# Kernel tuning notes

Hardware: AMD Instinct MI355X
Metric: run time of the kernel (lower is better)

## Reference

```python
import jax, jax.numpy as jnp
import numpy as np

B, C, H, W, NH = 4, 96, 256, 256, 4


def setup_inputs() -> dict:
    key = jax.random.key(0)
    ks = jax.random.split(key, 8)
    s = 0.05  # keep pre-activations well-scaled
    return {
        "x": jax.random.normal(ks[0], (B, C, H, W), jnp.float32),
        "ff": jax.random.normal(ks[1], (B, C, H, W), jnp.float32),
        "w_q": jax.random.normal(ks[2], (C, C, 1, 1), jnp.float32) * s,
        "w_kv": jax.random.normal(ks[3], (2 * C, C, 1, 1), jnp.float32) * s,
        "w_q_dw": jax.random.normal(ks[4], (C, 1, 3, 3), jnp.float32) * s,
        "w_kv_dw": jax.random.normal(ks[5], (2 * C, 1, 3, 3), jnp.float32) * s,
        "w_out": jax.random.normal(ks[6], (C, C, 1, 1), jnp.float32) * s,
        "temperature": jnp.ones((NH, 1, 1), jnp.float32),
    }


def _conv1x1(x, w):
    # pointwise conv == channel GEMM; w: [O, I, 1, 1]
    return jnp.einsum('bchw,oc->bohw', x, w[:, :, 0, 0])


def _dwconv3(x, w):
    # depthwise 3x3, padding=1; w: [C, 1, 3, 3]
    return jax.lax.conv_general_dilated(
        x, w, window_strides=(1, 1), padding='SAME',
        feature_group_count=x.shape[1],
        dimension_numbers=('NCHW', 'OIHW', 'NCHW'))


def _l2norm(t, eps=1e-12):
    # L2-normalize along last (HW) axis, torch F.normalize semantics
    n = jnp.sqrt(jnp.sum(t * t, axis=-1, keepdims=True))
    return t / jnp.maximum(n, eps)


def reference(x, ff, w_q, w_kv, w_q_dw, w_kv_dw, w_out, temperature):
    b, c, h, w = x.shape
    q = _dwconv3(_conv1x1(ff, w_q), w_q_dw)          # [B,C,H,W]
    kv = _dwconv3(_conv1x1(x, w_kv), w_kv_dw)        # [B,2C,H,W]
    k, v = jnp.split(kv, 2, axis=1)

    def heads(t):
        return t.reshape(b, NH, c // NH, h * w)       # [B,nh,c,HW]

    q = _l2norm(heads(q))
    k = _l2norm(heads(k))
    v = heads(v)
    # channel-wise (transposed) attention: [B,nh,c,c]
    attn = jax.nn.softmax(jnp.einsum('bhcn,bhdn->bhcd', q, k) * temperature, axis=-1)
    o = jnp.einsum('bhcd,bhdn->bhcn', attn, v).reshape(b, c, h, w)
    return _conv1x1(o, w_out)
```

## Files before the change

kernel.cpp:

```cpp
#include <hip/hip_runtime.h>
#include <hip/hip_bf16.h>
#include <hip/hip_fp16.h>

typedef unsigned int u32;
typedef unsigned short u16;
typedef _Float16 f16;

static constexpr int HWn = 65536;

typedef __attribute__((ext_vector_type(8))) f16 f16x8;
typedef __attribute__((ext_vector_type(2))) f16 f16x2;
typedef __attribute__((ext_vector_type(4))) float f32x4;

__device__ __forceinline__ float h2f(u16 u) {
    union { u16 s; f16 h; } z; z.s = u; return (float)z.h;
}
__device__ __forceinline__ u16 f2h(float f) {
    union { u16 s; f16 h; } z; z.h = (f16)f; return z.s;
}
__device__ __forceinline__ u32 pack2h(float a, float b) {
    union { u32 i; f16 h[2]; } z; z.h[0] = (f16)a; z.h[1] = (f16)b; return z.i;
}
__device__ __forceinline__ float hlo(u32 u) {
    union { u32 i; f16 h[2]; } z; z.i = u; return (float)z.h[0];
}
__device__ __forceinline__ float hhi(u32 u) {
    union { u32 i; f16 h[2]; } z; z.i = u; return (float)z.h[1];
}
__device__ __forceinline__ float sq2h(u32 a) {
    const float l = hlo(a), h = hhi(a);
    return fmaf(l, l, h * h);
}

#if defined(__has_builtin)
#if __has_builtin(__builtin_amdgcn_fdot2)
#define HAS_FDOT2 1
#endif
#endif
__device__ __forceinline__ float fdot2a(u32 a, u32 b, float c) {
#ifdef HAS_FDOT2
    union { u32 i; f16x2 h; } A, B; A.i = a; B.i = b;
    return __builtin_amdgcn_fdot2(A.h, B.h, c, false);
#else
    return fmaf(hlo(a), hlo(b), fmaf(hhi(a), hhi(b), c));
#endif
}

__device__ __forceinline__ int xoff(int px, int icb) {
    return px * 128 + (((icb ^ (px & 7) ^ ((px >> 3) & 7))) << 3);
}

__global__ __launch_bounds__(256) void k_prep_w(
    const float* __restrict__ wq, const float* __restrict__ wkv,
    u16* __restrict__ wf)
{
    const int i = blockIdx.x * 256 + threadIdx.x;
    if (i >= 288 * 96) return;
    const int row = i / 96, ic = i % 96;
    const float w = (row < 96) ? wq[row * 96 + ic] : wkv[(row - 96) * 96 + ic];
    wf[i] = f2h(w);
}

__global__ __launch_bounds__(256, 3) void k_conv_mfma(
    const float* __restrict__ ff, const float* __restrict__ x,
    const u16* __restrict__ wf,
    u16* __restrict__ qpre, u16* __restrict__ kvpre)
{
    const int b = blockIdx.z, sec = blockIdx.y;
    const int pxb = blockIdx.x * 256;
    const int tid = threadIdx.x;

    __shared__ __align__(16) u16 xs[16384];

    const float* src = (sec == 0 ? ff : x) + (size_t)b * 96 * HWn;
    const int icq = (tid >> 4) * 2;
    const int pxs = (tid & 15) * 8;
    const int lane = tid & 63;
    const int wv = tid >> 6;
    const int oc0 = (wv >> 1) * 48;
    const int pxw = (wv & 1) * 64;
    const int lr = lane & 15, lg = lane >> 4;

    float4 L[12];

    auto issue = [&](int px0) {
        #pragma unroll
        for (int p = 0; p < 3; ++p) {
            const float* rp0 = src + (size_t)(p * 32 + icq) * HWn + px0 + pxs;
            const float* rp1 = rp0 + HWn;
            L[p * 4 + 0] = *reinterpret_cast<const float4*>(rp0);
            L[p * 4 + 1] = *reinterpret_cast<const float4*>(rp0 + 4);
            L[p * 4 + 2] = *reinterpret_cast<const float4*>(rp1);
            L[p * 4 + 3] = *reinterpret_cast<const float4*>(rp1 + 4);
        }
    };
    auto stage = [&]() {
        #pragma unroll
        for (int p = 0; p < 3; ++p) {
            const int ic = p * 32 + icq;
            const int icb = ic >> 3, icl = ic & 7;
            const float e0[8] = {L[p*4+0].x, L[p*4+0].y, L[p*4+0].z, L[p*4+0].w,
                                 L[p*4+1].x, L[p*4+1].y, L[p*4+1].z, L[p*4+1].w};
            const float e1[8] = {L[p*4+2].x, L[p*4+2].y, L[p*4+2].z, L[p*4+2].w,
                                 L[p*4+3].x, L[p*4+3].y, L[p*4+3].z, L[p*4+3].w};
            #pragma unroll
            for (int j = 0; j < 8; ++j) {
                const int o = xoff(pxs + j, icb) + icl;
                *reinterpret_cast<u32*>(&xs[o]) = pack2h(e0[j], e1[j]);
            }
        }
    };
    auto compute = [&](int px0) {
        const int npass = (sec == 0) ? 1 : 2;
        #pragma unroll 1
        for (int kvs = 0; kvs < npass; ++kvs) {
            const u16* wh = wf + ((sec == 0) ? 0 : (96 + kvs * 96)) * 96;
            u16* dst = (sec == 0) ? (qpre + (size_t)b * 96 * HWn)
                                  : (kvpre + (size_t)b * 192 * HWn + (size_t)kvs * 96 * HWn);
            f32x4 acc[3][4];
            #pragma unroll
            for (int m = 0; m < 3; ++m)
                #pragma unroll
                for (int n = 0; n < 4; ++n)
                    acc[m][n] = (f32x4){0.f, 0.f, 0.f, 0.f};

            #pragma unroll 1
            for (int kt = 0; kt < 3; ++kt) {
                const int kb = kt * 32;
                f16x8 B[4];
                #pragma unroll
                for (int n = 0; n < 4; ++n)
                    B[n] = *(const f16x8*)(xs + xoff(pxw + n * 16 + lr, (kb >> 3) + lg));
                f16x8 A[3];
                #pragma unroll
                for (int m = 0; m < 3; ++m)
                    A[m] = *(const f16x8*)(wh + (oc0 + m * 16 + lr) * 96 + kb + lg * 8);
                #pragma unroll
                for (int m = 0; m < 3; ++m)
                    #pragma unroll
                    for (int n = 0; n < 4; ++n)
                        acc[m][n] = __builtin_amdgcn_mfma_f32_16x16x32_f16(A[m], B[n], acc[m][n], 0, 0, 0);
            }

            #pragma unroll
            for (int m = 0; m < 3; ++m) {
                #pragma unroll
                for (int i = 0; i < 4; ++i) {
                    const int oc = oc0 + m * 16 + lg * 4 + i;
                    u16* drow = dst + (size_t)oc * HWn + px0;
                    #pragma unroll
                    for (int n = 0; n < 4; ++n)
                        drow[pxw + n * 16 + lr] = f2h(acc[m][n][i]);
                }
            }
        }
    };

    issue(pxb);
    stage();
    __syncthreads();
    issue(pxb + 128);
    compute(pxb);
    __syncthreads();
    stage();
    __syncthreads();
    compute(pxb + 128);
}

__device__ __forceinline__ void row3tap(
    const uint4 m, u32 lv, u32 rv, u32 w01, u32 w2z, float* a)
{
    const u32 P0 = m.x, P1 = m.y, P2 = m.z, P3 = m.w;
    const u32 s0 = (lv >> 16) | (P0 << 16);
    const u32 s1 = (P0 >> 16) | (P1 << 16);
    const u32 s2 = (P1 >> 16) | (P2 << 16);
    const u32 s3 = (P2 >> 16) | (P3 << 16);
    const u32 s4 = (P3 >> 16) | (rv << 16);
    a[0] = fdot2a(w2z, s1, fdot2a(w01, s0, a[0]));
    a[1] = fdot2a(w2z, P1, fdot2a(w01, P0, a[1]));
    a[2] = fdot2a(w2z, s2, fdot2a(w01, s1, a[2]));
    a[3] = fdot2a(w2z, P2, fdot2a(w01, P1, a[3]));
    a[4] = fdot2a(w2z, s3, fdot2a(w01, s2, a[4]));
    a[5] = fdot2a(w2z, P3, fdot2a(w01, P2, a[5]));
    a[6] = fdot2a(w2z, s4, fdot2a(w01, s3, a[6]));
    a[7] = fdot2a(w2z, rv, fdot2a(w01, P3, a[7]));
}

__global__ __launch_bounds__(512) void k_dw_qk(
    const u16* __restrict__ qpre, const u16* __restrict__ kvpre,
    const float* __restrict__ wqdw, const float* __restrict__ wkvdw,
    float* __restrict__ ssq, float* __restrict__ Sg)
{
    const int bid = blockIdx.x;
    const int wg = (bid & 7) * 256 + (bid >> 3);
    const int b = wg >> 9;
    const int rem = wg & 511;
    const int y = rem >> 1;
    const int tx = (rem & 1) * 128;
    const int tid = threadIdx.x;
    const int lane = tid & 63;
    const int pq = tid >> 4;
    const int chunk = tid & 15;
    const int x0l = chunk * 8;
    const int xg = tx + x0l;

    const bool vr0 = (y > 0), vr2 = (y < 255);
    const bool le = (chunk == 0) && (xg > 0);
    const bool re = (chunk == 15) && (xg + 8 < 256);

    __shared__ __align__(16) u16 qs[96][136];
    __shared__ __align__(16) u16 ks[96][136];

    auto addr = [&](int it, const u16*& src, const float*& wp, int& c, int& seg) {
        const int p = it * 32 + pq;
        if (p < 96) { c = p;      src = qpre  + ((size_t)(b * 96 + c)) * HWn;  wp = wqdw  + c * 9; seg = 0; }
        else        { c = p - 96; src = kvpre + ((size_t)(b * 192 + c)) * HWn; wp = wkvdw + c * 9; seg = 1; }
    };
    auto issue = [&](const u16* src, uint4* m, u32* el, u32* er) {
        const uint4 z = make_uint4(0u, 0u, 0u, 0u);
        const u16* r0 = src + (y - 1) * 256 + xg;
        const u16* r1 = r0 + 256;
        const u16* r2 = r1 + 256;
        m[0] = vr0 ? *reinterpret_cast<const uint4*>(r0) : z;
        m[1] = *reinterpret_cast<const uint4*>(r1);
        m[2] = vr2 ? *reinterpret_cast<const uint4*>(r2) : z;
        el[0] = (le && vr0) ? ((u32)r0[-1] << 16) : 0u;  er[0] = (re && vr0) ? (u32)r0[8] : 0u;
        el[1] = le ? ((u32)r1[-1] << 16) : 0u;           er[1] = re ? (u32)r1[8] : 0u;
        el[2] = (le && vr2) ? ((u32)r2[-1] << 16) : 0u;  er[2] = (re && vr2) ? (u32)r2[8] : 0u;
    };

    const u16* srcC; const float* wpC; int cC, segC;
    addr(0, srcC, wpC, cC, segC);
    uint4 mcur[3]; u32 elc[3], erc[3];
    issue(srcC, mcur, elc, erc);

    #pragma unroll 1
    for (int it = 0; it < 6; ++it) {
        const u16* srcN; const float* wpN; int cN, segN;
        uint4 mnx[3]; u32 eln[3], ern[3];
        if (it < 5) {
            addr(it + 1, srcN, wpN, cN, segN);
            issue(srcN, mnx, eln, ern);
        }

        float a[8] = {0.f, 0.f, 0.f, 0.f, 0.f, 0.f, 0.f, 0.f};
        #pragma unroll
        for (int r = 0; r < 3; ++r) {
            const u32 w01 = pack2h(wpC[r * 3 + 0], wpC[r * 3 + 1]);
            const u32 w2z = pack2h(wpC[r * 3 + 2], 0.f);
            const u32 lvn = __shfl((int)mcur[r].w, (lane - 1) & 63);
            const u32 rvn = __shfl((int)mcur[r].x, (lane + 1) & 63);
            const u32 lv = (chunk == 0)  ? elc[r] : lvn;
            const u32 rv = (chunk == 15) ? erc[r] : rvn;
            row3tap(mcur[r], lv, rv, w01, w2z, a);
        }

        const uint4 o = make_uint4(pack2h(a[0], a[1]), pack2h(a[2], a[3]),
                                   pack2h(a[4], a[5]), pack2h(a[6], a[7]));
        if (segC == 0) *reinterpret_cast<uint4*>(&qs[cC][x0l]) = o;
        else           *reinterpret_cast<uint4*>(&ks[cC][x0l]) = o;

        if (it < 5) {
            #pragma unroll
            for (int r = 0; r < 3; ++r) { mcur[r] = mnx[r]; elc[r] = eln[r]; erc[r] = ern[r]; }
            wpC = wpN; cC = cN; segC = segN;
        }
    }
    __syncthreads();

    if (tid < 384) {
        const int half = tid >= 192;
        const int r = tid - half * 192;
        const uint4* rr = reinterpret_cast<const uint4*>(
            (r < 96 ? &qs[r][0] : &ks[r - 96][0]) + half * 64);
        float s = 0.f;
        #pragma unroll
        for (int pch = 0; pch < 8; ++pch) {
            const uint4 a = rr[pch];
            s += sq2h(a.x) + sq2h(a.y) + sq2h(a.z) + sq2h(a.w);
        }
        atomicAdd(ssq + b * 192 + r, s);
    }

    {
        const int w = tid >> 6;
        const int h = w & 3, mt = w >> 2;
        const int lr2 = lane & 15, lg2 = lane >> 4;
        const int ar = h * 24 + min(mt * 16 + lr2, 23);
        f32x4 acc2[2];
        acc2[0] = (f32x4){0.f, 0.f, 0.f, 0.f};
        acc2[1] = (f32x4){0.f, 0.f, 0.f, 0.f};
        #pragma unroll
        for (int ks4 = 0; ks4 < 4; ++ks4) {
            const f16x8 A = *(const f16x8*)(&qs[ar][ks4 * 32 + lg2 * 8]);
            #pragma unroll
            for (int nt = 0; nt < 2; ++nt) {
                const int bc = h * 24 + min(nt * 16 + lr2, 23);
                const f16x8 B = *(const f16x8*)(&ks[bc][ks4 * 32 + lg2 * 8]);
                acc2[nt] = __builtin_amdgcn_mfma_f32_16x16x32_f16(A, B, acc2[nt], 0, 0, 0);
            }
        }
        #pragma unroll
        for (int nt = 0; nt < 2; ++nt) {
            const int col = nt * 16 + lr2;
            #pragma unroll
            for (int reg = 0; reg < 4; ++reg) {
                const int row24 = mt * 16 + lg2 * 4 + reg;
                if (row24 < 24 && col < 24)
                    atomicAdd(Sg + b * 2304 + h * 576 + row24 * 24 + col, acc2[nt][reg]);
            }
        }
    }
}

__global__ __launch_bounds__(256) void k_attn_fold(
    const float* __restrict__ ssq, const float* __restrict__ S,
    const float* __restrict__ temp, const float* __restrict__ w_out,
    u16* __restrict__ mf)
{
    const int b = blockIdx.x;
    const int tid = threadIdx.x;
    __shared__ float rq[96], rk[96], att[2304];

    if (tid < 96) {
        rq[tid] = 1.f / fmaxf(sqrtf(ssq[b * 192 + tid]), 1e-12f);
    } else if (tid < 192) {
        const int c = tid - 96;
        rk[c] = 1.f / fmaxf(sqrtf(ssq[b * 192 + 96 + c]), 1e-12f);
    }
    __syncthreads();

    if (tid < 96) {
        const int h = tid / 24, i = tid % 24;
        const float tmp = temp[h];
        const float rqi = rq[h * 24 + i];
        float l[24];
        float m = -1e30f;
        #pragma unroll
        for (int j = 0; j < 24; ++j) {
            l[j] = S[b * 2304 + (h * 24 + i) * 24 + j] * rqi * rk[h * 24 + j] * tmp;
            m = fmaxf(m, l[j]);
        }
        float ssum = 0.f;
        #pragma unroll
        for (int j = 0; j < 24; ++j) { l[j] = expf(l[j] - m); ssum += l[j]; }
        const float inv = 1.f / ssum;
        #pragma unroll
        for (int j = 0; j < 24; ++j) att[(h * 24 + i) * 24 + j] = l[j] * inv;
    }
    __syncthreads();

    for (int k = 0; k < 36; ++k) {
        const int id = k * 256 + tid;
        const int dg = id / 96, oc = id % 96;
        const int h = dg / 24, d24 = dg % 24;
        float s = 0.f;
        #pragma unroll
        for (int i = 0; i < 24; ++i) {
            s += w_out[oc * 96 + h * 24 + i] * att[(h * 24 + i) * 24 + d24];
        }
        mf[b * 9216 + oc * 96 + dg] = f2h(s);
    }
}

__global__ __launch_bounds__(256, 4) void k_v_out(
    const u16* __restrict__ kvpre, const float* __restrict__ wkvdw,
    const u16* __restrict__ mf, float* __restrict__ out)
{
    const int bid = blockIdx.x;
    const int wg = (bid & 7) * 256 + (bid >> 3);
    const int b = wg >> 9;
    const int rem = wg & 511;
    const int y = rem >> 1;
    const int tx = (rem & 1) * 128;
    const int tid = threadIdx.x;
    const int lane = tid & 63;
    const int slot = tid >> 4;
    const int chunk = tid & 15;
    const int x0l = chunk * 8;
    const int xg = tx + x0l;

    const bool vr0 = (y > 0), vr2 = (y < 255);
    const bool le = (chunk == 0) && (xg > 0);
    const bool re = (chunk == 15) && (xg + 8 < 256);

    __shared__ __align__(16) u16 xt[16384];

    auto issue = [&](int it, uint4* m0, uint4* m1, u32* e0l, u32* e0r, u32* e1l, u32* e1r) {
        const int dg = (it * 16 + slot) * 2;
        const u16* s0 = kvpre + ((size_t)(b * 192 + 96 + dg)) * HWn + (y - 1) * 256 + xg;
        const u16* s1 = s0 + HWn;
        const uint4 z = make_uint4(0u, 0u, 0u, 0u);
        m0[0] = vr0 ? *reinterpret_cast<const uint4*>(s0)       : z;
        m0[1] =       *reinterpret_cast<const uint4*>(s0 + 256);
        m0[2] = vr2 ? *reinterpret_cast<const uint4*>(s0 + 512) : z;
        m1[0] = vr0 ? *reinterpret_cast<const uint4*>(s1)       : z;
        m1[1] =       *reinterpret_cast<const uint4*>(s1 + 256);
        m1[2] = vr2 ? *reinterpret_cast<const uint4*>(s1 + 512) : z;
        e0l[0] = (le && vr0) ? ((u32)s0[-1] << 16) : 0u;   e0r[0] = (re && vr0) ? (u32)s0[8] : 0u;
        e0l[1] = le ? ((u32)s0[255] << 16) : 0u;           e0r[1] = re ? (u32)s0[264] : 0u;
        e0l[2] = (le && vr2) ? ((u32)s0[511] << 16) : 0u;  e0r[2] = (re && vr2) ? (u32)s0[520] : 0u;
        e1l[0] = (le && vr0) ? ((u32)s1[-1] << 16) : 0u;   e1r[0] = (re && vr0) ? (u32)s1[8] : 0u;
        e1l[1] = le ? ((u32)s1[255] << 16) : 0u;           e1r[1] = re ? (u32)s1[264] : 0u;
        e1l[2] = (le && vr2) ? ((u32)s1[511] << 16) : 0u;  e1r[2] = (re && vr2) ? (u32)s1[520] : 0u;
    };

    uint4 m0c[3], m1c[3]; u32 e0lc[3], e0rc[3], e1lc[3], e1rc[3];
    issue(0, m0c, m1c, e0lc, e0rc, e1lc, e1rc);

    #pragma unroll 1
    for (int it = 0; it < 3; ++it) {
        uint4 m0n[3], m1n[3]; u32 e0ln[3], e0rn[3], e1ln[3], e1rn[3];
        if (it < 2) issue(it + 1, m0n, m1n, e0ln, e0rn, e1ln, e1rn);

        const int dg = (it * 16 + slot) * 2;
        const float* wp0 = wkvdw + (96 + dg) * 9;
        const float* wp1 = wp0 + 9;

        float a0[8] = {0.f, 0.f, 0.f, 0.f, 0.f, 0.f, 0.f, 0.f};
        float a1[8] = {0.f, 0.f, 0.f, 0.f, 0.f, 0.f, 0.f, 0.f};
        #pragma unroll
        for (int r = 0; r < 3; ++r) {
            {
                const u32 w01 = pack2h(wp0[r * 3 + 0], wp0[r * 3 + 1]);
                const u32 w2z = pack2h(wp0[r * 3 + 2], 0.f);
                const u32 lvn = __shfl((int)m0c[r].w, (lane - 1) & 63);
                const u32 rvn = __shfl((int)m0c[r].x, (lane + 1) & 63);
                const u32 lv = (chunk == 0)  ? e0lc[r] : lvn;
                const u32 rv = (chunk == 15) ? e0rc[r] : rvn;
                row3tap(m0c[r], lv, rv, w01, w2z, a0);
            }
            {
                const u32 w01 = pack2h(wp1[r * 3 + 0], wp1[r * 3 + 1]);
                const u32 w2z = pack2h(wp1[r * 3 + 2], 0.f);
                const u32 lvn = __shfl((int)m1c[r].w, (lane - 1) & 63);
                const u32 rvn = __shfl((int)m1c[r].x, (lane + 1) & 63);
                const u32 lv = (chunk == 0)  ? e1lc[r] : lvn;
                const u32 rv = (chunk == 15) ? e1rc[r] : rvn;
                row3tap(m1c[r], lv, rv, w01, w2z, a1);
            }
        }

        const int icb = dg >> 3, icl = dg & 7;
        #pragma unroll
        for (int j = 0; j < 8; ++j) {
            *reinterpret_cast<u32*>(&xt[xoff(x0l + j, icb) + icl]) = pack2h(a0[j], a1[j]);
        }

        if (it < 2) {
            #pragma unroll
            for (int r = 0; r < 3; ++r) {
                m0c[r] = m0n[r]; m1c[r] = m1n[r];
                e0lc[r] = e0ln[r]; e0rc[r] = e0rn[r];
                e1lc[r] = e1ln[r]; e1rc[r] = e1rn[r];
            }
        }
    }
    __syncthreads();

    const u16* mh = mf + b * 9216;
    const int wv = tid >> 6;
    const int oc0 = (wv >> 1) * 48;
    const int pxw = (wv & 1) * 64;
    const int lr = lane & 15, lg = lane >> 4;

    f32x4 acc[3][4];
    #pragma unroll
    for (int m = 0; m < 3; ++m)
        #pragma unroll
        for (int n = 0; n < 4; ++n)
            acc[m][n] = (f32x4){0.f, 0.f, 0.f, 0.f};

    #pragma unroll 1
    for (int kt = 0; kt < 3; ++kt) {
        const int kb = kt * 32;
        f16x8 B[4];
        #pragma unroll
        for (int n = 0; n < 4; ++n)
            B[n] = *(const f16x8*)(xt + xoff(pxw + n * 16 + lr, (kb >> 3) + lg));
        f16x8 A[3];
        #pragma unroll
        for (int m = 0; m < 3; ++m)
            A[m] = *(const f16x8*)(mh + (oc0 + m * 16 + lr) * 96 + kb + lg * 8);
        #pragma unroll
        for (int m = 0; m < 3; ++m)
            #pragma unroll
            for (int n = 0; n < 4; ++n)
                acc[m][n] = __builtin_amdgcn_mfma_f32_16x16x32_f16(A[m], B[n], acc[m][n], 0, 0, 0);
    }

    #pragma unroll
    for (int m = 0; m < 3; ++m) {
        #pragma unroll
        for (int i = 0; i < 4; ++i) {
            const int oc = oc0 + m * 16 + lg * 4 + i;
            float* drow = out + ((size_t)(b * 96 + oc)) * HWn + y * 256 + tx;
            #pragma unroll
            for (int n = 0; n < 4; ++n)
                drow[pxw + n * 16 + lr] = acc[m][n][i];
        }
    }
}

extern "C" void kernel_launch(void* const* d_in, const int* in_sizes, int n_in,
                              void* d_out, int out_size, void* d_ws, size_t ws_size,
                              hipStream_t stream) {
    (void)in_sizes; (void)n_in; (void)out_size; (void)ws_size;
    const float* x      = (const float*)d_in[0];
    const float* ff     = (const float*)d_in[1];
    const float* w_q    = (const float*)d_in[2];
    const float* w_kv   = (const float*)d_in[3];
    const float* w_q_dw = (const float*)d_in[4];
    const float* w_kv_dw= (const float*)d_in[5];
    const float* w_out  = (const float*)d_in[6];
    const float* temp   = (const float*)d_in[7];
    float* out = (float*)d_out;

    char* ws = (char*)d_ws;
    u16* qpre   = (u16*)(ws);
    u16* kvpre  = (u16*)(ws + 50331648);
    float* ssq  = (float*)(ws + 150994944);
    float* S    = (float*)(ws + 150998016);
    u16* wf     = (u16*)(ws + 151034880);
    u16* mf     = (u16*)(ws + 151090176);

    hipMemsetAsync(ws + 150994944, 0, 3072 + 36864, stream);

    k_prep_w<<<108, 256, 0, stream>>>(w_q, w_kv, wf);
    k_conv_mfma<<<dim3(256, 2, 4), 256, 0, stream>>>(ff, x, wf, qpre, kvpre);
    k_dw_qk<<<dim3(2048), 512, 0, stream>>>(qpre, kvpre, w_q_dw, w_kv_dw, ssq, S);
    k_attn_fold<<<4, 256, 0, stream>>>(ssq, S, temp, w_out, mf);
    k_v_out<<<dim3(2048), 256, 0, stream>>>(kvpre, w_kv_dw, mf, out);
}
```

Before: 257.0 us.

## Shrink conv and depthwise tiles, drop software prefetch, raise occupancy

The pointwise-conv kernel now processes 64 pixels per block instead of two 128-pixel halves with register prefetch. It stages fp32 inputs into half the shared memory and launches four times as many blocks with a higher occupancy hint. The depthwise/QK kernel now handles a 64-wide tile with 64 channels per iteration instead of 128-wide with 32. It drops the next-iteration prefetch and doubles the grid. The intent is to hide latency with more resident waves rather than explicit pipelining, at the cost of more blocks, more atomics on ssq/S and more halo reloads.

```diff
diff --git a/kernel.cpp b/kernel.cpp
--- a/kernel.cpp
+++ b/kernel.cpp
@@ -61,110 +61,85 @@
     wf[i] = f2h(w);
 }
 
-__global__ __launch_bounds__(256, 3) void k_conv_mfma(
+__global__ __launch_bounds__(256, 6) void k_conv_mfma(
     const float* __restrict__ ff, const float* __restrict__ x,
     const u16* __restrict__ wf,
     u16* __restrict__ qpre, u16* __restrict__ kvpre)
 {
     const int b = blockIdx.z, sec = blockIdx.y;
-    const int pxb = blockIdx.x * 256;
+    const int px0 = blockIdx.x * 64;
     const int tid = threadIdx.x;
 
-    __shared__ __align__(16) u16 xs[16384];
+    __shared__ __align__(16) u16 xs[8192];
 
     const float* src = (sec == 0 ? ff : x) + (size_t)b * 96 * HWn;
-    const int icq = (tid >> 4) * 2;
-    const int pxs = (tid & 15) * 8;
+
+    const int ics = tid >> 3;
+    const int pxs = (tid & 7) * 8;
+    #pragma unroll
+    for (int p = 0; p < 3; ++p) {
+        const int ic = p * 32 + ics;
+        const float* rp = src + (size_t)ic * HWn + px0 + pxs;
+        const float4 a0 = *reinterpret_cast<const float4*>(rp);
+        const float4 a1 = *reinterpret_cast<const float4*>(rp + 4);
+        const int icb = ic >> 3, icl = ic & 7;
+        const float e[8] = {a0.x, a0.y, a0.z, a0.w, a1.x, a1.y, a1.z, a1.w};
+        #pragma unroll
+        for (int j = 0; j < 8; ++j)
+            xs[xoff(pxs + j, icb) + icl] = f2h(e[j]);
+    }
+    __syncthreads();
+
     const int lane = tid & 63;
     const int wv = tid >> 6;
     const int oc0 = (wv >> 1) * 48;
-    const int pxw = (wv & 1) * 64;
+    const int pxw = (wv & 1) * 32;
     const int lr = lane & 15, lg = lane >> 4;
 
-    float4 L[12];
-
-    auto issue = [&](int px0) {
-        #pragma unroll
-        for (int p = 0; p < 3; ++p) {
-            const float* rp0 = src + (size_t)(p * 32 + icq) * HWn + px0 + pxs;
-            const float* rp1 = rp0 + HWn;
-            L[p * 4 + 0] = *reinterpret_cast<const float4*>(rp0);
-            L[p * 4 + 1] = *reinterpret_cast<const float4*>(rp0 + 4);
-            L[p * 4 + 2] = *reinterpret_cast<const float4*>(rp1);
-            L[p * 4 + 3] = *reinterpret_cast<const float4*>(rp1 + 4);
-        }
-    };
-    auto stage = [&]() {
-        #pragma unroll
-        for (int p = 0; p < 3; ++p) {
-            const int ic = p * 32 + icq;
-            const int icb = ic >> 3, icl = ic & 7;
-            const float e0[8] = {L[p*4+0].x, L[p*4+0].y, L[p*4+0].z, L[p*4+0].w,
-                                 L[p*4+1].x, L[p*4+1].y, L[p*4+1].z, L[p*4+1].w};
-            const float e1[8] = {L[p*4+2].x, L[p*4+2].y, L[p*4+2].z, L[p*4+2].w,
-                                 L[p*4+3].x, L[p*4+3].y, L[p*4+3].z, L[p*4+3].w};
-            #pragma unroll
-            for (int j = 0; j < 8; ++j) {
-                const int o = xoff(pxs + j, icb) + icl;
-                *reinterpret_cast<u32*>(&xs[o]) = pack2h(e0[j], e1[j]);
-            }
-        }
-    };
-    auto compute = [&](int px0) {
-        const int npass = (sec == 0) ? 1 : 2;
+    const int npass = (sec == 0) ? 1 : 2;
+    #pragma unroll 1
+    for (int kvs = 0; kvs < npass; ++kvs) {
+        const u16* wh = wf + ((sec == 0) ? 0 : (96 + kvs * 96)) * 96;
+        u16* dst = (sec == 0) ? (qpre + (size_t)b * 96 * HWn)
+                              : (kvpre + (size_t)b * 192 * HWn + (size_t)kvs * 96 * HWn);
+
+        f32x4 acc[3][2];
+        #pragma unroll
+        for (int m = 0; m < 3; ++m)
+            #pragma unroll
+            for (int n = 0; n < 2; ++n)
+                acc[m][n] = (f32x4){0.f, 0.f, 0.f, 0.f};
+
         #pragma unroll 1
-        for (int kvs = 0; kvs < npass; ++kvs) {
-            const u16* wh = wf + ((sec == 0) ? 0 : (96 + kvs * 96)) * 96;
-            u16* dst = (sec == 0) ? (qpre + (size_t)b * 96 * HWn)
-                                  : (kvpre + (size_t)b * 192 * HWn + (size_t)kvs * 96 * HWn);
-            f32x4 acc[3][4];
+        for (int kt = 0; kt < 3; ++kt) {
+            const int kb = kt * 32;
+            f16x8 B[2];
+            #pragma unroll
+            for (int n = 0; n < 2; ++n)
+                B[n] = *(const f16x8*)(xs + xoff(pxw + n * 16 + lr, (kb >> 3) + lg));
+            f16x8 A[3];
+            #pragma unroll
+            for (int m = 0; m < 3; ++m)
+                A[m] = *(const f16x8*)(wh + (oc0 + m * 16 + lr) * 96 + kb + lg * 8);
             #pragma unroll
             for (int m = 0; m < 3; ++m)
                 #pragma unroll
-                for (int n = 0; n < 4; ++n)
-                    acc[m][n] = (f32x4){0.f, 0.f, 0.f, 0.f};
-
-            #pragma unroll 1
-            for (int kt = 0; kt < 3; ++kt) {
-                const int kb = kt * 32;
-                f16x8 B[4];
+                for (int n = 0; n < 2; ++n)
+                    acc[m][n] = __builtin_amdgcn_mfma_f32_16x16x32_f16(A[m], B[n], acc[m][n], 0, 0, 0);
+        }
+
+        #pragma unroll
+        for (int m = 0; m < 3; ++m) {
+            #pragma unroll
+            for (int i = 0; i < 4; ++i) {
+                const int oc = oc0 + m * 16 + lg * 4 + i;
+                u16* drow = dst + (size_t)oc * HWn + px0;
                 #pragma unroll
-                for (int n = 0; n < 4; ++n)
-                    B[n] = *(const f16x8*)(xs + xoff(pxw + n * 16 + lr, (kb >> 3) + lg));
-                f16x8 A[3];
-                #pragma unroll
-                for (int m = 0; m < 3; ++m)
-                    A[m] = *(const f16x8*)(wh + (oc0 + m * 16 + lr) * 96 + kb + lg * 8);
-                #pragma unroll
-                for (int m = 0; m < 3; ++m)
-                    #pragma unroll
-                    for (int n = 0; n < 4; ++n)
-                        acc[m][n] = __builtin_amdgcn_mfma_f32_16x16x32_f16(A[m], B[n], acc[m][n], 0, 0, 0);
-            }
-
-            #pragma unroll
-            for (int m = 0; m < 3; ++m) {
-                #pragma unroll
-                for (int i = 0; i < 4; ++i) {
-                    const int oc = oc0 + m * 16 + lg * 4 + i;
-                    u16* drow = dst + (size_t)oc * HWn + px0;
-                    #pragma unroll
-                    for (int n = 0; n < 4; ++n)
-                        drow[pxw + n * 16 + lr] = f2h(acc[m][n][i]);
-                }
-            }
-        }
-    };
-
-    issue(pxb);
-    stage();
-    __syncthreads();
-    issue(pxb + 128);
-    compute(pxb);
-    __syncthreads();
-    stage();
-    __syncthreads();
-    compute(pxb + 128);
+                for (int n = 0; n < 2; ++n)
+                    drow[pxw + n * 16 + lr] = f2h(acc[m][n][i]);
+            }
+        }
+    }
 }
 
 __device__ __forceinline__ void row3tap(
@@ -186,100 +161,80 @@
     a[7] = fdot2a(w2z, rv, fdot2a(w01, P3, a[7]));
 }
 
-__global__ __launch_bounds__(512) void k_dw_qk(
+__global__ __launch_bounds__(512, 8) void k_dw_qk(
     const u16* __restrict__ qpre, const u16* __restrict__ kvpre,
     const float* __restrict__ wqdw, const float* __restrict__ wkvdw,
     float* __restrict__ ssq, float* __restrict__ Sg)
 {
     const int bid = blockIdx.x;
-    const int wg = (bid & 7) * 256 + (bid >> 3);
-    const int b = wg >> 9;
-    const int rem = wg & 511;
-    const int y = rem >> 1;
-    const int tx = (rem & 1) * 128;
+    const int wg = (bid & 7) * 512 + (bid >> 3);
+    const int b = wg >> 10;
+    const int rem = wg & 1023;
+    const int y = rem >> 2;
+    const int tx = (rem & 3) * 64;
     const int tid = threadIdx.x;
     const int lane = tid & 63;
-    const int pq = tid >> 4;
-    const int chunk = tid & 15;
+    const int pq = tid >> 3;
+    const int chunk = tid & 7;
     const int x0l = chunk * 8;
     const int xg = tx + x0l;
 
     const bool vr0 = (y > 0), vr2 = (y < 255);
     const bool le = (chunk == 0) && (xg > 0);
-    const bool re = (chunk == 15) && (xg + 8 < 256);
-
-    __shared__ __align__(16) u16 qs[96][136];
-    __shared__ __align__(16) u16 ks[96][136];
-
-    auto addr = [&](int it, const u16*& src, const float*& wp, int& c, int& seg) {
-        const int p = it * 32 + pq;
+    const bool re = (chunk == 7) && (xg + 8 < 256);
+
+    __shared__ __align__(16) u16 qs[96][72];
+    __shared__ __align__(16) u16 ks[96][72];
+
+    #pragma unroll 1
+    for (int it = 0; it < 3; ++it) {
+        const int p = it * 64 + pq;
+        const u16* src; const float* wp; int c, seg;
         if (p < 96) { c = p;      src = qpre  + ((size_t)(b * 96 + c)) * HWn;  wp = wqdw  + c * 9; seg = 0; }
         else        { c = p - 96; src = kvpre + ((size_t)(b * 192 + c)) * HWn; wp = wkvdw + c * 9; seg = 1; }
-    };
-    auto issue = [&](const u16* src, uint4* m, u32* el, u32* er) {
-        const uint4 z = make_uint4(0u, 0u, 0u, 0u);
+
         const u16* r0 = src + (y - 1) * 256 + xg;
         const u16* r1 = r0 + 256;
         const u16* r2 = r1 + 256;
+        const uint4 z = make_uint4(0u, 0u, 0u, 0u);
+        uint4 m[3];
         m[0] = vr0 ? *reinterpret_cast<const uint4*>(r0) : z;
         m[1] = *reinterpret_cast<const uint4*>(r1);
         m[2] = vr2 ? *reinterpret_cast<const uint4*>(r2) : z;
+        u32 el[3], er[3];
         el[0] = (le && vr0) ? ((u32)r0[-1] << 16) : 0u;  er[0] = (re && vr0) ? (u32)r0[8] : 0u;
         el[1] = le ? ((u32)r1[-1] << 16) : 0u;           er[1] = re ? (u32)r1[8] : 0u;
         el[2] = (le && vr2) ? ((u32)r2[-1] << 16) : 0u;  er[2] = (re && vr2) ? (u32)r2[8] : 0u;
-    };
-
-    const u16* srcC; const float* wpC; int cC, segC;
-    addr(0, srcC, wpC, cC, segC);
-    uint4 mcur[3]; u32 elc[3], erc[3];
-    issue(srcC, mcur, elc, erc);
-
-    #pragma unroll 1
-    for (int it = 0; it < 6; ++it) {
-        const u16* srcN; const float* wpN; int cN, segN;
-        uint4 mnx[3]; u32 eln[3], ern[3];
-        if (it < 5) {
-            addr(it + 1, srcN, wpN, cN, segN);
-            issue(srcN, mnx, eln, ern);
-        }
 
         float a[8] = {0.f, 0.f, 0.f, 0.f, 0.f, 0.f, 0.f, 0.f};
         #pragma unroll
         for (int r = 0; r < 3; ++r) {
-            const u32 w01 = pack2h(wpC[r * 3 + 0], wpC[r * 3 + 1]);
-            const u32 w2z = pack2h(wpC[r * 3 + 2], 0.f);
-            const u32 lvn = __shfl((int)mcur[r].w, (lane - 1) & 63);
-            const u32 rvn = __shfl((int)mcur[r].x, (lane + 1) & 63);
-            const u32 lv = (chunk == 0)  ? elc[r] : lvn;
-            const u32 rv = (chunk == 15) ? erc[r] : rvn;
-            row3tap(mcur[r], lv, rv, w01, w2z, a);
+            const u32 w01 = pack2h(wp[r * 3 + 0], wp[r * 3 + 1]);
+            const u32 w2z = pack2h(wp[r * 3 + 2], 0.f);
+            const u32 lvn = __shfl((int)m[r].w, (lane - 1) & 63);
+            const u32 rvn = __shfl((int)m[r].x, (lane + 1) & 63);
+            const u32 lv = (chunk == 0) ? el[r] : lvn;
+            const u32 rv = (chunk == 7) ? er[r] : rvn;
+            row3tap(m[r], lv, rv, w01, w2z, a);
         }
 
         const uint4 o = make_uint4(pack2h(a[0], a[1]), pack2h(a[2], a[3]),
                                    pack2h(a[4], a[5]), pack2h(a[6], a[7]));
-        if (segC == 0) *reinterpret_cast<uint4*>(&qs[cC][x0l]) = o;
-        else           *reinterpret_cast<uint4*>(&ks[cC][x0l]) = o;
-
-        if (it < 5) {
-            #pragma unroll
-            for (int r = 0; r < 3; ++r) { mcur[r] = mnx[r]; elc[r] = eln[r]; erc[r] = ern[r]; }
-            wpC = wpN; cC = cN; segC = segN;
-        }
+        if (seg == 0) *reinterpret_cast<uint4*>(&qs[c][x0l]) = o;
+        else          *reinterpret_cast<uint4*>(&ks[c][x0l]) = o;
     }
     __syncthreads();
 
-    if (tid < 384) {
-        const int half = tid >= 192;
-        const int r = tid - half * 192;
+    if (tid < 192) {
         const uint4* rr = reinterpret_cast<const uint4*>(
-            (r < 96 ? &qs[r][0] : &ks[r - 96][0]) + half * 64);
+            tid < 96 ? &qs[tid][0] : &ks[tid - 96][0]);
         float s = 0.f;
         #pragma unroll
         for (int pch = 0; pch < 8; ++pch) {
             const uint4 a = rr[pch];
             s += sq2h(a.x) + sq2h(a.y) + sq2h(a.z) + sq2h(a.w);
         }
-        atomicAdd(ssq + b * 192 + r, s);
+        atomicAdd(ssq + b * 192 + tid, s);
     }
 
     {
@@ -291,7 +246,7 @@
         acc2[0] = (f32x4){0.f, 0.f, 0.f, 0.f};
         acc2[1] = (f32x4){0.f, 0.f, 0.f, 0.f};
         #pragma unroll
-        for (int ks4 = 0; ks4 < 4; ++ks4) {
+        for (int ks4 = 0; ks4 < 2; ++ks4) {
             const f16x8 A = *(const f16x8*)(&qs[ar][ks4 * 32 + lg2 * 8]);
             #pragma unroll
             for (int nt = 0; nt < 2; ++nt) {
@@ -527,8 +482,8 @@
     hipMemsetAsync(ws + 150994944, 0, 3072 + 36864, stream);
 
     k_prep_w<<<108, 256, 0, stream>>>(w_q, w_kv, wf);
-    k_conv_mfma<<<dim3(256, 2, 4), 256, 0, stream>>>(ff, x, wf, qpre, kvpre);
-    k_dw_qk<<<dim3(2048), 512, 0, stream>>>(qpre, kvpre, w_q_dw, w_kv_dw, ssq, S);
+    k_conv_mfma<<<dim3(1024, 2, 4), 256, 0, stream>>>(ff, x, wf, qpre, kvpre);
+    k_dw_qk<<<dim3(4096), 512, 0, stream>>>(qpre, kvpre, w_q_dw, w_kv_dw, ssq, S);
     k_attn_fold<<<4, 256, 0, stream>>>(ssq, S, temp, w_out, mf);
     k_v_out<<<dim3(2048), 256, 0, stream>>>(kvpre, w_kv_dw, mf, out);
 }
```

Measured after the change: 301.6 us. 1.17x slower.

## Process batches sequentially and fuse attention fold into the output kernel

Applied to the files above, without the earlier changes.

The host now loops over the batch, launching conv, depthwise/QK and V-output kernels once per batch. The q/kv intermediate buffers shrink to one batch's worth so they can stay resident in cache between stages. The separate softmax/fold kernel is removed: every k_v_out block recomputes the softmax and the w_out·attn matrix into shared memory. The trade-off is redundant per-block fold work, more and smaller launches, and extra LDS use, with a lower occupancy hint in launch bounds.

```diff
diff --git a/kernel.cpp b/kernel.cpp
--- a/kernel.cpp
+++ b/kernel.cpp
@@ -62,17 +62,17 @@
 }
 
 __global__ __launch_bounds__(256, 3) void k_conv_mfma(
-    const float* __restrict__ ff, const float* __restrict__ x,
+    const float* __restrict__ ffb, const float* __restrict__ xb,
     const u16* __restrict__ wf,
     u16* __restrict__ qpre, u16* __restrict__ kvpre)
 {
-    const int b = blockIdx.z, sec = blockIdx.y;
+    const int sec = blockIdx.y;
     const int pxb = blockIdx.x * 256;
     const int tid = threadIdx.x;
 
     __shared__ __align__(16) u16 xs[16384];
 
-    const float* src = (sec == 0 ? ff : x) + (size_t)b * 96 * HWn;
+    const float* src = (sec == 0) ? ffb : xb;
     const int icq = (tid >> 4) * 2;
     const int pxs = (tid & 15) * 8;
     const int lane = tid & 63;
@@ -115,8 +115,7 @@
         #pragma unroll 1
         for (int kvs = 0; kvs < npass; ++kvs) {
             const u16* wh = wf + ((sec == 0) ? 0 : (96 + kvs * 96)) * 96;
-            u16* dst = (sec == 0) ? (qpre + (size_t)b * 96 * HWn)
-                                  : (kvpre + (size_t)b * 192 * HWn + (size_t)kvs * 96 * HWn);
+            u16* dst = (sec == 0) ? qpre : (kvpre + (size_t)kvs * 96 * HWn);
             f32x4 acc[3][4];
             #pragma unroll
             for (int m = 0; m < 3; ++m)
@@ -192,11 +191,9 @@
     float* __restrict__ ssq, float* __restrict__ Sg)
 {
     const int bid = blockIdx.x;
-    const int wg = (bid & 7) * 256 + (bid >> 3);
-    const int b = wg >> 9;
-    const int rem = wg & 511;
-    const int y = rem >> 1;
-    const int tx = (rem & 1) * 128;
+    const int wg = (bid & 7) * 64 + (bid >> 3);
+    const int y = wg >> 1;
+    const int tx = (wg & 1) * 128;
     const int tid = threadIdx.x;
     const int lane = tid & 63;
     const int pq = tid >> 4;
@@ -213,8 +210,8 @@
 
     auto addr = [&](int it, const u16*& src, const float*& wp, int& c, int& seg) {
         const int p = it * 32 + pq;
-        if (p < 96) { c = p;      src = qpre  + ((size_t)(b * 96 + c)) * HWn;  wp = wqdw  + c * 9; seg = 0; }
-        else        { c = p - 96; src = kvpre + ((size_t)(b * 192 + c)) * HWn; wp = wkvdw + c * 9; seg = 1; }
+        if (p < 96) { c = p;      src = qpre  + (size_t)c * HWn;  wp = wqdw  + c * 9; seg = 0; }
+        else        { c = p - 96; src = kvpre + (size_t)c * HWn;  wp = wkvdw + c * 9; seg = 1; }
     };
     auto issue = [&](const u16* src, uint4* m, u32* el, u32* er) {
         const uint4 z = make_uint4(0u, 0u, 0u, 0u);
@@ -279,7 +276,7 @@
             const uint4 a = rr[pch];
             s += sq2h(a.x) + sq2h(a.y) + sq2h(a.z) + sq2h(a.w);
         }
-        atomicAdd(ssq + b * 192 + r, s);
+        atomicAdd(ssq + r, s);
     }
 
     {
@@ -307,72 +304,22 @@
             for (int reg = 0; reg < 4; ++reg) {
                 const int row24 = mt * 16 + lg2 * 4 + reg;
                 if (row24 < 24 && col < 24)
-                    atomicAdd(Sg + b * 2304 + h * 576 + row24 * 24 + col, acc2[nt][reg]);
-            }
-        }
-    }
-}
-
-__global__ __launch_bounds__(256) void k_attn_fold(
-    const float* __restrict__ ssq, const float* __restrict__ S,
+                    atomicAdd(Sg + h * 576 + row24 * 24 + col, acc2[nt][reg]);
+            }
+        }
+    }
+}
+
+__global__ __launch_bounds__(256, 3) void k_v_out(
+    const u16* __restrict__ kvpre, const float* __restrict__ wkvdw,
+    const float* __restrict__ Sg, const float* __restrict__ ssq,
     const float* __restrict__ temp, const float* __restrict__ w_out,
-    u16* __restrict__ mf)
-{
-    const int b = blockIdx.x;
-    const int tid = threadIdx.x;
-    __shared__ float rq[96], rk[96], att[2304];
-
-    if (tid < 96) {
-        rq[tid] = 1.f / fmaxf(sqrtf(ssq[b * 192 + tid]), 1e-12f);
-    } else if (tid < 192) {
-        const int c = tid - 96;
-        rk[c] = 1.f / fmaxf(sqrtf(ssq[b * 192 + 96 + c]), 1e-12f);
-    }
-    __syncthreads();
-
-    if (tid < 96) {
-        const int h = tid / 24, i = tid % 24;
-        const float tmp = temp[h];
-        const float rqi = rq[h * 24 + i];
-        float l[24];
-        float m = -1e30f;
-        #pragma unroll
-        for (int j = 0; j < 24; ++j) {
-            l[j] = S[b * 2304 + (h * 24 + i) * 24 + j] * rqi * rk[h * 24 + j] * tmp;
-            m = fmaxf(m, l[j]);
-        }
-        float ssum = 0.f;
-        #pragma unroll
-        for (int j = 0; j < 24; ++j) { l[j] = expf(l[j] - m); ssum += l[j]; }
-        const float inv = 1.f / ssum;
-        #pragma unroll
-        for (int j = 0; j < 24; ++j) att[(h * 24 + i) * 24 + j] = l[j] * inv;
-    }
-    __syncthreads();
-
-    for (int k = 0; k < 36; ++k) {
-        const int id = k * 256 + tid;
-        const int dg = id / 96, oc = id % 96;
-        const int h = dg / 24, d24 = dg % 24;
-        float s = 0.f;
-        #pragma unroll
-        for (int i = 0; i < 24; ++i) {
-            s += w_out[oc * 96 + h * 24 + i] * att[(h * 24 + i) * 24 + d24];
-        }
-        mf[b * 9216 + oc * 96 + dg] = f2h(s);
-    }
-}
-
-__global__ __launch_bounds__(256, 4) void k_v_out(
-    const u16* __restrict__ kvpre, const float* __restrict__ wkvdw,
-    const u16* __restrict__ mf, float* __restrict__ out)
+    float* __restrict__ outb)
 {
     const int bid = blockIdx.x;
-    const int wg = (bid & 7) * 256 + (bid >> 3);
-    const int b = wg >> 9;
-    const int rem = wg & 511;
-    const int y = rem >> 1;
-    const int tx = (rem & 1) * 128;
+    const int wg = (bid & 7) * 64 + (bid >> 3);
+    const int y = wg >> 1;
+    const int tx = (wg & 1) * 128;
     const int tid = threadIdx.x;
     const int lane = tid & 63;
     const int slot = tid >> 4;
@@ -385,10 +332,50 @@
     const bool re = (chunk == 15) && (xg + 8 < 256);
 
     __shared__ __align__(16) u16 xt[16384];
+    __shared__ float rq[96], rk[96];
+    __shared__ __align__(16) u16 mfs[96 * 100];
+
+    float* att = reinterpret_cast<float*>(xt);
+    if (tid < 192) {
+        const float r = 1.f / fmaxf(sqrtf(ssq[tid]), 1e-12f);
+        if (tid < 96) rq[tid] = r; else rk[tid - 96] = r;
+    }
+    __syncthreads();
+    if (tid < 96) {
+        const int h = tid / 24, i = tid % 24;
+        const float tmp = temp[h];
+        const float rqi = rq[tid];
+        float l[24];
+        float m = -1e30f;
+        #pragma unroll
+        for (int j = 0; j < 24; ++j) {
+            l[j] = Sg[(h * 24 + i) * 24 + j] * rqi * rk[h * 24 + j] * tmp;
+            m = fmaxf(m, l[j]);
+        }
+        float ssum = 0.f;
+        #pragma unroll
+        for (int j = 0; j < 24; ++j) { l[j] = expf(l[j] - m); ssum += l[j]; }
+        const float inv = 1.f / ssum;
+        #pragma unroll
+        for (int j = 0; j < 24; ++j) att[(h * 24 + i) * 24 + j] = l[j] * inv;
+    }
+    __syncthreads();
+    #pragma unroll 1
+    for (int k2 = 0; k2 < 36; ++k2) {
+        const int id = k2 * 256 + tid;
+        const int dg = id / 96, oc = id % 96;
+        const int h = dg / 24, d24 = dg % 24;
+        float s = 0.f;
+        #pragma unroll
+        for (int i = 0; i < 24; ++i)
+            s += w_out[oc * 96 + h * 24 + i] * att[(h * 24 + i) * 24 + d24];
+        mfs[oc * 100 + dg] = f2h(s);
+    }
+    __syncthreads();
 
     auto issue = [&](int it, uint4* m0, uint4* m1, u32* e0l, u32* e0r, u32* e1l, u32* e1r) {
         const int dg = (it * 16 + slot) * 2;
-        const u16* s0 = kvpre + ((size_t)(b * 192 + 96 + dg)) * HWn + (y - 1) * 256 + xg;
+        const u16* s0 = kvpre + ((size_t)(96 + dg)) * HWn + (y - 1) * 256 + xg;
         const u16* s1 = s0 + HWn;
         const uint4 z = make_uint4(0u, 0u, 0u, 0u);
         m0[0] = vr0 ? *reinterpret_cast<const uint4*>(s0)       : z;
@@ -458,7 +445,6 @@
     }
     __syncthreads();
 
-    const u16* mh = mf + b * 9216;
     const int wv = tid >> 6;
     const int oc0 = (wv >> 1) * 48;
     const int pxw = (wv & 1) * 64;
@@ -481,7 +467,7 @@
         f16x8 A[3];
         #pragma unroll
         for (int m = 0; m < 3; ++m)
-            A[m] = *(const f16x8*)(mh + (oc0 + m * 16 + lr) * 96 + kb + lg * 8);
+            A[m] = *(const f16x8*)(mfs + (oc0 + m * 16 + lr) * 100 + kb + lg * 8);
         #pragma unroll
         for (int m = 0; m < 3; ++m)
             #pragma unroll
@@ -494,7 +480,7 @@
         #pragma unroll
         for (int i = 0; i < 4; ++i) {
             const int oc = oc0 + m * 16 + lg * 4 + i;
-            float* drow = out + ((size_t)(b * 96 + oc)) * HWn + y * 256 + tx;
+            float* drow = outb + (size_t)oc * HWn + y * 256 + tx;
             #pragma unroll
             for (int n = 0; n < 4; ++n)
                 drow[pxw + n * 16 + lr] = acc[m][n][i];
@@ -518,17 +504,20 @@
 
     char* ws = (char*)d_ws;
     u16* qpre   = (u16*)(ws);
-    u16* kvpre  = (u16*)(ws + 50331648);
-    float* ssq  = (float*)(ws + 150994944);
-    float* S    = (float*)(ws + 150998016);
-    u16* wf     = (u16*)(ws + 151034880);
-    u16* mf     = (u16*)(ws + 151090176);
-
-    hipMemsetAsync(ws + 150994944, 0, 3072 + 36864, stream);
-
+    u16* kvpre  = (u16*)(ws + 12582912);
+    float* S    = (float*)(ws + 37748736);
+    float* ssq  = (float*)(ws + 37785600);
+    u16* wf     = (u16*)(ws + 37788672);
+
+    hipMemsetAsync(ws + 37748736, 0, 36864 + 3072, stream);
     k_prep_w<<<108, 256, 0, stream>>>(w_q, w_kv, wf);
-    k_conv_mfma<<<dim3(256, 2, 4), 256, 0, stream>>>(ff, x, wf, qpre, kvpre);
-    k_dw_qk<<<dim3(2048), 512, 0, stream>>>(qpre, kvpre, w_q_dw, w_kv_dw, ssq, S);
-    k_attn_fold<<<4, 256, 0, stream>>>(ssq, S, temp, w_out, mf);
-    k_v_out<<<dim3(2048), 256, 0, stream>>>(kvpre, w_kv_dw, mf, out);
-}
+
+    for (int b = 0; b < 4; ++b) {
+        const size_t po = (size_t)b * 96 * HWn;
+        k_conv_mfma<<<dim3(256, 2), 256, 0, stream>>>(ff + po, x + po, wf, qpre, kvpre);
+        k_dw_qk<<<512, 512, 0, stream>>>(qpre, kvpre, w_q_dw, w_kv_dw,
+                                         ssq + b * 192, S + b * 2304);
+        k_v_out<<<512, 256, 0, stream>>>(kvpre, w_kv_dw, S + b * 2304, ssq + b * 192,
+                                         temp, w_out, out + po);
+    }
+}
```

Result: slower. 544.1 us (+111.7%).
